# Performance work log

Hardware: AMD Instinct MI355X
Metric: run time of the kernel (lower is better)

The kernel has to match this reference:

```python
import jax, jax.numpy as jnp
import numpy as np

C, N, H = 24, 1536, 40          # n_clusters, max_cluster_size, max_hull_vertices
SEP_W, T_PEN, R_PEN = 1.0, 0.1, 1.0
EPS = 1e-8


def setup_inputs() -> dict:
    rng = np.random.default_rng(0)
    medoids = rng.uniform(0.0, 100.0, (C, 2)).astype(np.float32)
    pts = np.zeros((C, N, 2), np.float32)
    pmask = np.zeros((C, N), bool)
    hulls = np.zeros((C, H, 2), np.float32)
    hmask = np.zeros((C, H), bool)
    for i in range(C):  # loop over fixed small n_clusters (setup only)
        n = int(rng.integers(N // 2, N + 1))
        pts[i, :n] = medoids[i] + rng.normal(0.0, 5.0, (n, 2))
        pmask[i, :n] = True
        h = int(rng.integers(16, H + 1))
        ang = np.sort(rng.uniform(0.0, 2.0 * np.pi, h))
        r = rng.uniform(6.0, 12.0)
        v = (medoids[i] + r * np.stack([np.cos(ang), np.sin(ang)], 1)).astype(np.float32)
        hulls[i, :h] = v
        hulls[i, h:] = v[-1]  # repeat last vertex -> padding edges have zero length
        hmask[i, :h] = True
    k1, k2 = jax.random.split(jax.random.key(0))
    return {
        'padded_clusters': jnp.asarray(pts),
        'padded_hulls': jnp.asarray(hulls),
        'medoids': jnp.asarray(medoids),
        'rotation_angles': 0.1 * jax.random.normal(k1, (C,), jnp.float32),
        'translations': jax.random.normal(k2, (C, 2), jnp.float32),
        'cluster_masks': jnp.asarray(pmask),
        'hull_masks': jnp.asarray(hmask),
    }


def _transform(x, medoids, angles, trans):
    # rotation about medoid, then translate: matches apply_transformations_vectorized
    c, s = jnp.cos(angles), jnp.sin(angles)
    # torch bmm(points, R) with R[k] = [[cos, sin], [-sin, cos]]
    R = jnp.stack([jnp.stack([c, s], -1), jnp.stack([-s, c], -1)], -2)  # (C,2,2)
    centered = x - medoids[:, None, :]
    return jnp.einsum('cnd,cde->cne', centered, R) + (medoids + trans)[:, None, :]


def reference(padded_clusters, padded_hulls, medoids, rotation_angles, translations,
              cluster_masks, hull_masks):
    pts = _transform(padded_clusters, medoids, rotation_angles, translations)  # (C,N,2)
    hul = _transform(padded_hulls, medoids, rotation_angles, translations)     # (C,H,2)

    p1 = hul
    p2 = jnp.roll(hul, -1, axis=1)
    edges = p2 - p1                                   # (C,H,2)
    elen_raw = jnp.linalg.norm(edges, axis=-1)        # (C,H)
    elen = elen_raw + EPS
    evalid = elen_raw > 1e-6                          # skip zero-length padding edges

    ex, ey = edges[..., 0], edges[..., 1]
    c0 = ex * p1[..., 1] - ey * p1[..., 0]            # (C,H)
    px, py = pts[..., 0], pts[..., 1]
    cross = (ex[None, :, None, :] * py[:, None, :, None]
             - ey[None, :, None, :] * px[:, None, :, None]
             - c0[None, :, None, :])                  # (C,C,N,H)
    signed = cross / elen[None, :, None, :]

    v = evalid[None, :, None, :]
    all_pos = jnp.all(jnp.where(v, signed >= -EPS, True), axis=-1)
    all_neg = jnp.all(jnp.where(v, signed <= EPS, True), axis=-1)
    inside = all_pos | all_neg                        # (C,C,N)
    min_abs = jnp.min(jnp.where(v, jnp.abs(signed), jnp.inf), axis=-1)
    viol = jnp.where(inside, jax.nn.sigmoid(min_abs), 0.0)

    hull_ok = jnp.sum(hull_masks, -1) >= 3            # hull_mask.sum() < 3 -> zeros
    offdiag = ~jnp.eye(C, dtype=bool)                 # own hull excluded
    m = cluster_masks[:, None, :] & offdiag[:, :, None] & hull_ok[None, :, None]
    sep = jnp.sum(jnp.where(m, viol, 0.0))

    return (SEP_W * sep
            + T_PEN * jnp.sum(translations ** 2)
            + R_PEN * jnp.sum(rotation_angles ** 2))
```

## Files before the change

### kernel.cpp

```cpp
#include <hip/hip_runtime.h>
#include <math.h>

#define NC    24
#define NPTS  1536
#define NH    40
#define FEPS  1e-8f
#define GROUPS 4
#define JPG    6

__device__ __forceinline__ int mask_fmt(const void* m) {
    int w = ((const int*)m)[0];
    if (w == 1) return 1;
    if (w == 0x3f800000) return 2;
    return 0;
}
__device__ __forceinline__ bool mask_at(const void* m, int idx, int fmt) {
    if (fmt == 1) return ((const int*)m)[idx] != 0;
    if (fmt == 2) return ((const float*)m)[idx] != 0.0f;
    return ((const unsigned char*)m)[idx] != 0;
}

__global__ __launch_bounds__(1024)
void prep_kernel(const float* __restrict__ hulls, const float* __restrict__ med,
                 const float* __restrict__ ang, const float* __restrict__ trans,
                 const void* __restrict__ hmask,
                 float4* __restrict__ edges, int* __restrict__ hok,
                 float* __restrict__ out)
{
    const int tid = threadIdx.x;
    if (tid < NC * NH) {
        const int j = tid / NH, h = tid % NH;
        float sj, cj;
        __sincosf(ang[j], &sj, &cj);
        const float mx = med[2*j], my = med[2*j+1];
        const float tx = trans[2*j], ty = trans[2*j+1];
        const int hn = (h + 1 == NH) ? 0 : h + 1;
        const float x1 = hulls[(j*NH + h )*2], y1 = hulls[(j*NH + h )*2 + 1];
        const float x2 = hulls[(j*NH + hn)*2], y2 = hulls[(j*NH + hn)*2 + 1];
        const float cx1 = x1 - mx, cy1 = y1 - my;
        const float p1x = cx1*cj - cy1*sj + mx + tx;
        const float p1y = cx1*sj + cy1*cj + my + ty;
        const float cx2 = x2 - mx, cy2 = y2 - my;
        const float p2x = cx2*cj - cy2*sj + mx + tx;
        const float p2y = cx2*sj + cy2*cj + my + ty;
        const float ex = p2x - p1x, ey = p2y - p1y;
        const float el = sqrtf(ex*ex + ey*ey);
        const float inv = (el > 1e-6f) ? 1.0f / (el + FEPS) : 0.0f;
        const float c0 = ex*p1y - ey*p1x;
        edges[tid] = make_float4(ex, ey, c0, inv);
    } else if (tid < NC * NH + NC) {
        const int j = tid - NC * NH;
        const int hfmt = mask_fmt(hmask);
        int cnt = 0;
        for (int h = 0; h < NH; ++h) cnt += mask_at(hmask, j*NH + h, hfmt) ? 1 : 0;
        hok[j] = (cnt >= 3) ? 1 : 0;
    } else if (tid == 1023) {
        float pen = 0.f;
        for (int c = 0; c < NC; ++c) {
            const float tx = trans[2*c], ty = trans[2*c+1], a = ang[c];
            pen += 0.1f * (tx*tx + ty*ty) + 1.0f * (a*a);
        }
        atomicAdd(out, pen);
    }
}

__global__ __launch_bounds__(256)
void eval_kernel(const float* __restrict__ pts, const float* __restrict__ med,
                 const float* __restrict__ ang, const float* __restrict__ trans,
                 const void* __restrict__ cmask,
                 const float4* __restrict__ edges, const int* __restrict__ hok,
                 float* __restrict__ out)
{
    const int tid = threadIdx.x;
    const int i = blockIdx.y;
    const int z = blockIdx.z;

    __shared__ float4 s_e[JPG * NH];
    __shared__ int    s_ok[JPG];
    __shared__ float  s_part[4];

    if (tid < JPG * NH) s_e[tid] = edges[z * JPG * NH + tid];
    if (tid < JPG)      s_ok[tid] = hok[z * JPG + tid];
    __syncthreads();

    const int n = blockIdx.x * 256 + tid;
    const int cfmt = mask_fmt(cmask);
    const bool pm = mask_at(cmask, i*NPTS + n, cfmt);
    float si, ci;
    __sincosf(ang[i], &si, &ci);
    const float mx = med[2*i], my = med[2*i+1];
    const float tx = trans[2*i], ty = trans[2*i+1];
    const float x = pts[(i*NPTS + n)*2 + 0];
    const float y = pts[(i*NPTS + n)*2 + 1];
    const float cx = x - mx, cy = y - my;
    const float px = cx*ci - cy*si + mx + tx;
    const float py = cx*si + cy*ci + my + ty;

    float acc = 0.f;
    for (int g = 0; g < JPG; ++g) {
        const int j = z * JPG + g;
        if (j == i || !s_ok[g]) continue;
        bool allpos = true, allneg = true;
        float minabs = INFINITY;
#pragma unroll
        for (int h = 0; h < NH; ++h) {
            const float4 e = s_e[g*NH + h];
            const float cross = fmaf(e.x, py, -fmaf(e.y, px, e.z));
            const float sgn = cross * e.w;
            allpos = allpos && (sgn >= -FEPS);
            allneg = allneg && (sgn <=  FEPS);
            minabs = fminf(minabs, (e.w > 0.f) ? fabsf(sgn) : INFINITY);
        }
        if (allpos || allneg)
            acc += 1.0f / (1.0f + __expf(-minabs));
    }
    if (!pm) acc = 0.f;

#pragma unroll
    for (int off = 32; off > 0; off >>= 1)
        acc += __shfl_down(acc, off, 64);
    const int lane = tid & 63, wid = tid >> 6;
    if (lane == 0) s_part[wid] = acc;
    __syncthreads();
    if (tid == 0) atomicAdd(out, s_part[0] + s_part[1] + s_part[2] + s_part[3]);
}

extern "C" void kernel_launch(void* const* d_in, const int* in_sizes, int n_in,
                              void* d_out, int out_size, void* d_ws, size_t ws_size,
                              hipStream_t stream) {
    const float* pts   = (const float*)d_in[0];
    const float* hulls = (const float*)d_in[1];
    const float* med   = (const float*)d_in[2];
    const float* ang   = (const float*)d_in[3];
    const float* trans = (const float*)d_in[4];
    const void*  cmask = d_in[5];
    const void*  hmask = d_in[6];
    float* out = (float*)d_out;

    float4* edges = (float4*)d_ws;
    int*    hok   = (int*)((char*)d_ws + NC*NH*sizeof(float4));

    hipMemsetAsync(out, 0, sizeof(float), stream);
    prep_kernel<<<1, 1024, 0, stream>>>(hulls, med, ang, trans, hmask, edges, hok, out);
    dim3 grid(NPTS / 256, NC, GROUPS);
    eval_kernel<<<grid, dim3(256, 1, 1), 0, stream>>>(pts, med, ang, trans, cmask,
                                                      edges, hok, out);
}
```

Measured before the change: 90.57 us.

## Fuse hull-edge prep into eval kernel and replace atomics with partials reduction

Each eval block now computes its own six hulls' transformed edge coefficients and hull-validity flags directly into shared memory, so the separate prep kernel and its global round trip are gone. The memset and per-block atomicAdd are replaced by per-block partial sums written to the workspace, which a small finish kernel reduces and combines with the penalty terms. Launch count stays at two (memset+prep+eval becomes eval+finish), and each block repeats a small amount of edge computation. The final sum is also deterministic now.

```diff
diff --git a/kernel.cpp b/kernel.cpp
--- a/kernel.cpp
+++ b/kernel.cpp
@@ -1,12 +1,14 @@
 #include <hip/hip_runtime.h>
 #include <math.h>
 
-#define NC    24
-#define NPTS  1536
-#define NH    40
-#define FEPS  1e-8f
+#define NC     24
+#define NPTS   1536
+#define NH     40
+#define FEPS   1e-8f
 #define GROUPS 4
 #define JPG    6
+#define BX     (NPTS / 256)
+#define NPART  (BX * NC * GROUPS)
 
 __device__ __forceinline__ int mask_fmt(const void* m) {
     int w = ((const int*)m)[0];
@@ -20,16 +22,23 @@
     return ((const unsigned char*)m)[idx] != 0;
 }
 
-__global__ __launch_bounds__(1024)
-void prep_kernel(const float* __restrict__ hulls, const float* __restrict__ med,
-                 const float* __restrict__ ang, const float* __restrict__ trans,
-                 const void* __restrict__ hmask,
-                 float4* __restrict__ edges, int* __restrict__ hok,
-                 float* __restrict__ out)
+__global__ __launch_bounds__(256)
+void eval_kernel(const float* __restrict__ pts, const float* __restrict__ hulls,
+                 const float* __restrict__ med, const float* __restrict__ ang,
+                 const float* __restrict__ trans, const void* __restrict__ cmask,
+                 const void* __restrict__ hmask, float* __restrict__ partials)
 {
     const int tid = threadIdx.x;
-    if (tid < NC * NH) {
-        const int j = tid / NH, h = tid % NH;
+    const int i = blockIdx.y;
+    const int z = blockIdx.z;
+
+    __shared__ float4 s_e[JPG * NH];
+    __shared__ int    s_ok[JPG];
+    __shared__ float  s_part[4];
+
+    if (tid < JPG * NH) {
+        const int g = tid / NH, h = tid % NH;
+        const int j = z * JPG + g;
         float sj, cj;
         __sincosf(ang[j], &sj, &cj);
         const float mx = med[2*j], my = med[2*j+1];
@@ -47,40 +56,15 @@
         const float el = sqrtf(ex*ex + ey*ey);
         const float inv = (el > 1e-6f) ? 1.0f / (el + FEPS) : 0.0f;
         const float c0 = ex*p1y - ey*p1x;
-        edges[tid] = make_float4(ex, ey, c0, inv);
-    } else if (tid < NC * NH + NC) {
-        const int j = tid - NC * NH;
+        s_e[tid] = make_float4(ex, ey, c0, inv);
+    } else if (tid < JPG * NH + JPG) {
+        const int g = tid - JPG * NH;
+        const int j = z * JPG + g;
         const int hfmt = mask_fmt(hmask);
         int cnt = 0;
         for (int h = 0; h < NH; ++h) cnt += mask_at(hmask, j*NH + h, hfmt) ? 1 : 0;
-        hok[j] = (cnt >= 3) ? 1 : 0;
-    } else if (tid == 1023) {
-        float pen = 0.f;
-        for (int c = 0; c < NC; ++c) {
-            const float tx = trans[2*c], ty = trans[2*c+1], a = ang[c];
-            pen += 0.1f * (tx*tx + ty*ty) + 1.0f * (a*a);
-        }
-        atomicAdd(out, pen);
+        s_ok[g] = (cnt >= 3) ? 1 : 0;
     }
-}
-
-__global__ __launch_bounds__(256)
-void eval_kernel(const float* __restrict__ pts, const float* __restrict__ med,
-                 const float* __restrict__ ang, const float* __restrict__ trans,
-                 const void* __restrict__ cmask,
-                 const float4* __restrict__ edges, const int* __restrict__ hok,
-                 float* __restrict__ out)
-{
-    const int tid = threadIdx.x;
-    const int i = blockIdx.y;
-    const int z = blockIdx.z;
-
-    __shared__ float4 s_e[JPG * NH];
-    __shared__ int    s_ok[JPG];
-    __shared__ float  s_part[4];
-
-    if (tid < JPG * NH) s_e[tid] = edges[z * JPG * NH + tid];
-    if (tid < JPG)      s_ok[tid] = hok[z * JPG + tid];
     __syncthreads();
 
     const int n = blockIdx.x * 256 + tid;
@@ -122,7 +106,31 @@
     const int lane = tid & 63, wid = tid >> 6;
     if (lane == 0) s_part[wid] = acc;
     __syncthreads();
-    if (tid == 0) atomicAdd(out, s_part[0] + s_part[1] + s_part[2] + s_part[3]);
+    if (tid == 0)
+        partials[(z * NC + i) * BX + blockIdx.x] =
+            s_part[0] + s_part[1] + s_part[2] + s_part[3];
+}
+
+__global__ __launch_bounds__(64)
+void finish_kernel(const float* __restrict__ partials, const float* __restrict__ ang,
+                   const float* __restrict__ trans, float* __restrict__ out)
+{
+    const int lane = threadIdx.x;
+    float s = 0.f;
+#pragma unroll
+    for (int k = 0; k < NPART / 64; ++k)
+        s += partials[lane * (NPART / 64) + k];
+#pragma unroll
+    for (int off = 32; off > 0; off >>= 1)
+        s += __shfl_xor(s, off, 64);
+    if (lane == 0) {
+        float pen = 0.f;
+        for (int c = 0; c < NC; ++c) {
+            const float tx = trans[2*c], ty = trans[2*c+1], a = ang[c];
+            pen += 0.1f * (tx*tx + ty*ty) + 1.0f * (a*a);
+        }
+        out[0] = s + pen;
+    }
 }
 
 extern "C" void kernel_launch(void* const* d_in, const int* in_sizes, int n_in,
@@ -135,14 +143,11 @@
     const float* trans = (const float*)d_in[4];
     const void*  cmask = d_in[5];
     const void*  hmask = d_in[6];
-    float* out = (float*)d_out;
+    float* out      = (float*)d_out;
+    float* partials = (float*)d_ws;
 
-    float4* edges = (float4*)d_ws;
-    int*    hok   = (int*)((char*)d_ws + NC*NH*sizeof(float4));
-
-    hipMemsetAsync(out, 0, sizeof(float), stream);
-    prep_kernel<<<1, 1024, 0, stream>>>(hulls, med, ang, trans, hmask, edges, hok, out);
-    dim3 grid(NPTS / 256, NC, GROUPS);
-    eval_kernel<<<grid, dim3(256, 1, 1), 0, stream>>>(pts, med, ang, trans, cmask,
-                                                      edges, hok, out);
+    dim3 grid(BX, NC, GROUPS);
+    eval_kernel<<<grid, dim3(256, 1, 1), 0, stream>>>(pts, hulls, med, ang, trans,
+                                                      cmask, hmask, partials);
+    finish_kernel<<<1, 64, 0, stream>>>(partials, ang, trans, out);
 }
```

Result: slower. 92.91 us (+2.6%).
